# Optimization experiments

Measured on AMD Instinct MI355X. Metric: run time of the kernel, lower is better.

## Reference

```python
import jax, jax.numpy as jnp
import numpy as np

RADIUS = 0.12
K = 32  # neighbors per ball


def setup_inputs() -> dict:
    key = jax.random.key(0)
    ks = jax.random.split(key, 12)
    B, N, M, C = 4, 4096, 4096, 128
    anchor_xyzs = jax.random.uniform(ks[0], (B, N, 3), dtype=jnp.float32)
    neighbor = jax.random.uniform(ks[1], (B, M, 3), dtype=jnp.float32)
    s3 = 1.0 / np.sqrt(3.0)
    sC = 1.0 / np.sqrt(C)
    Wq = jax.random.uniform(ks[2], (3, C), jnp.float32, -s3, s3)
    bq = jax.random.uniform(ks[3], (C,), jnp.float32, -s3, s3)
    Wk = jax.random.uniform(ks[4], (3, C), jnp.float32, -s3, s3)
    bk = jax.random.uniform(ks[5], (C,), jnp.float32, -s3, s3)
    Wd = jax.random.uniform(ks[6], (3, C), jnp.float32, -s3, s3)
    bd = jax.random.uniform(ks[7], (C,), jnp.float32, -s3, s3)
    Wa = jax.random.uniform(ks[8], (C, C), jnp.float32, -sC, sC)
    ba = jax.random.uniform(ks[9], (C,), jnp.float32, -sC, sC)
    return {"anchor_xyzs": anchor_xyzs, "neighbor": neighbor,
            "Wq": Wq, "bq": bq, "Wk": Wk, "bk": bk,
            "Wd": Wd, "bd": bd, "Wa": Wa, "ba": ba}


def ball_query(anchor, neighbor, radius, k):
    """pointnet2-style ball query: first k neighbor indices (in original order)
    with sqdist < radius^2; slots beyond the found count are padded with the
    first found index (index 0 if none found). Returns (B, N, k) int32."""
    # (B, N, M) pairwise squared distances
    sqd = jnp.sum((anchor[:, :, None, :] - neighbor[:, None, :, :]) ** 2, axis=-1)
    mask = sqd < radius * radius
    # stable sort keys: valid (0) before invalid (1) -> first-k valid indices in order
    order = jnp.argsort((~mask).astype(jnp.int32), axis=-1, stable=True)
    idx = order[..., :k]                                # (B, N, k)
    cnt = jnp.sum(mask, axis=-1)                        # (B, N)
    slot_valid = jnp.arange(k) < cnt[..., None]
    idx = jnp.where(slot_valid, idx, idx[..., :1])
    return idx.astype(jnp.int32)


def reference(anchor_xyzs, neighbor, Wq, bq, Wk, bk, Wd, bd, Wa, ba):
    B, N, _ = anchor_xyzs.shape
    bidx = jnp.arange(B)[:, None, None]
    # QKV-style projections of coordinates
    Q = anchor_xyzs @ Wq + bq                           # (B, N, C)
    neighbor_k = neighbor @ Wk + bk                     # (B, M, C)
    # ball query + gather
    idx = ball_query(anchor_xyzs, neighbor, RADIUS, K)  # (B, N, K)
    neighbor_grouped = neighbor[bidx, idx]              # (B, N, K, 3)
    features_K = neighbor_k[bidx, idx]                  # (B, N, K, C)
    # distance encoding
    dis = (anchor_xyzs[:, :, None, :] - neighbor_grouped) @ Wd + bd  # (B, N, K, C)
    # attention weight: softmax over channel dim (dim=-1, as in the torch code)
    logits = (Q[:, :, None, :] - features_K) @ Wa + ba  # (B, N, K, C)
    attention_weight = jax.nn.softmax(logits, axis=-1)
    # max-pool over the K neighbor axis
    attention = jnp.max(dis * attention_weight, axis=2)  # (B, N, C)
    return attention
```

## Files before the change

### kernel.cpp

```cpp
#include <hip/hip_runtime.h>
#include <math.h>

#define BDIM 4
#define NDIM 4096
#define MDIM 4096
#define CDIM 128
#define KSEL 32
#define NCELL 64
#define CAP 128

typedef float v2f __attribute__((ext_vector_type(2)));

#define PRE_BYTES (7 * CDIM * 4)
#define STARTS_BYTES ((NCELL + 1) * BDIM * 4)
#define PTS4_OFF (PRE_BYTES + STARTS_BYTES)
#define WS_NEEDED (PTS4_OFF + (size_t)BDIM * MDIM * 16)

__device__ __forceinline__ float exp2_hw(float x) {
    float r;
    asm("v_exp_f32 %0, %1" : "=v"(r) : "v"(x));
    return r;
}

template <int CTRL, int MASK>
__device__ __forceinline__ float dpp_add(float x) {
    const int r = __builtin_amdgcn_update_dpp(0, __float_as_int(x), CTRL, MASK, 0xF, true);
    return x + __int_as_float(r);
}
#define DPP_QUAD_XOR1 0xB1
#define DPP_QUAD_XOR2 0x4E
#define DPP_ROW_HALF_MIRROR 0x141
#define DPP_ROW_MIRROR      0x140
#define DPP_ROW_BCAST15     0x142
#define DPP_ROW_BCAST31     0x143

__device__ __forceinline__ int rank_before(unsigned long long mk) {
    return __builtin_amdgcn_mbcnt_hi((unsigned)(mk >> 32),
                                     __builtin_amdgcn_mbcnt_lo((unsigned)mk, 0));
}

__device__ __forceinline__ int cell_of(float v) {
    int c = (int)(v * 4.0f);
    return c < 0 ? 0 : (c > 3 ? 3 : c);
}

__device__ __forceinline__ v2f splat(float x) { v2f r; r.x = x; r.y = x; return r; }

__device__ __forceinline__ v2f pk_fma(v2f a, v2f b, v2f c) {
    return __builtin_elementwise_fma(a, b, c);
}

struct LaneW {
    v2f wqa0, wqa1, wqa2;
    v2f nka0, nka1, nka2;
    v2f cav;
    v2f wd0, wd1, wd2, bdv;
};

__device__ __forceinline__ void load_lane_weights(LaneW& P, const float* pre,
                                                  const float* Wd, const float* bd, int lane) {
    const v2f* pre2 = (const v2f*)pre;
    const v2f* wdp  = (const v2f*)Wd;
    const v2f* bdp  = (const v2f*)bd;
    P.wqa0 = pre2[0 * 64 + lane]; P.wqa1 = pre2[1 * 64 + lane]; P.wqa2 = pre2[2 * 64 + lane];
    P.nka0 = pre2[3 * 64 + lane]; P.nka1 = pre2[4 * 64 + lane]; P.nka2 = pre2[5 * 64 + lane];
    P.cav  = pre2[6 * 64 + lane];
    P.wd0 = wdp[0 * 64 + lane]; P.wd1 = wdp[1 * 64 + lane]; P.wd2 = wdp[2 * 64 + lane];
    P.bdv = bdp[lane];
}

__device__ __forceinline__ void fold_one(int i, const float* Wq, const float* bq,
                                         const float* Wk, const float* bk,
                                         const float* Wa, const float* ba,
                                         float* pre) {
    const double LOG2E = 1.4426950408889634074;
    const int r = i >> 7, c = i & (CDIM - 1);
    if (r < 3) {
        double s0 = 0, s1 = 0, s2 = 0, s3 = 0;
        for (int k = 0; k < CDIM; k += 4) {
            s0 += (double)Wq[r * CDIM + k + 0] * (double)Wa[(k + 0) * CDIM + c];
            s1 += (double)Wq[r * CDIM + k + 1] * (double)Wa[(k + 1) * CDIM + c];
            s2 += (double)Wq[r * CDIM + k + 2] * (double)Wa[(k + 2) * CDIM + c];
            s3 += (double)Wq[r * CDIM + k + 3] * (double)Wa[(k + 3) * CDIM + c];
        }
        pre[r * CDIM + c] = (float)(((s0 + s1) + (s2 + s3)) * LOG2E);
    } else if (r < 6) {
        const int rr = r - 3;
        double s0 = 0, s1 = 0, s2 = 0, s3 = 0;
        for (int k = 0; k < CDIM; k += 4) {
            s0 += (double)Wk[rr * CDIM + k + 0] * (double)Wa[(k + 0) * CDIM + c];
            s1 += (double)Wk[rr * CDIM + k + 1] * (double)Wa[(k + 1) * CDIM + c];
            s2 += (double)Wk[rr * CDIM + k + 2] * (double)Wa[(k + 2) * CDIM + c];
            s3 += (double)Wk[rr * CDIM + k + 3] * (double)Wa[(k + 3) * CDIM + c];
        }
        pre[r * CDIM + c] = (float)(((s0 + s1) + (s2 + s3)) * (-LOG2E));
    } else {
        double s = (double)ba[c];
        for (int k = 0; k < CDIM; ++k)
            s += ((double)bq[k] - (double)bk[k]) * (double)Wa[k * CDIM + c];
        pre[6 * CDIM + c] = (float)(s * LOG2E);
    }
}

__launch_bounds__(1024)
__global__ void setup_kernel(const float* __restrict__ neighbor,
                             const float* __restrict__ Wq, const float* __restrict__ bq,
                             const float* __restrict__ Wk, const float* __restrict__ bk,
                             const float* __restrict__ Wa, const float* __restrict__ ba,
                             float* __restrict__ pre,
                             int* __restrict__ starts,
                             float4* __restrict__ pts4,
                             const int do_bins) {
    const int blk = blockIdx.x;
    const int t = threadIdx.x;
    if (do_bins && blk < BDIM) {
        __shared__ int cnts[NCELL];
        __shared__ int curs[NCELL];
        if (t < NCELL) cnts[t] = 0;
        __syncthreads();
        const float* nbb = neighbor + (size_t)blk * MDIM * 3;
        float px[4], py[4], pz[4];
        int cell[4];
        #pragma unroll
        for (int k = 0; k < 4; ++k) {
            const int i = t + k * 1024;
            const float x = nbb[3 * i], y = nbb[3 * i + 1], z = nbb[3 * i + 2];
            px[k] = x; py[k] = y; pz[k] = z;
            cell[k] = (cell_of(z) * 4 + cell_of(y)) * 4 + cell_of(x);
            atomicAdd(&cnts[cell[k]], 1);
        }
        __syncthreads();
        if (t < NCELL) {
            const int v = cnts[t];
            int inc = v;
            #pragma unroll
            for (int off = 1; off < 64; off <<= 1) {
                const int u = __shfl_up(inc, off);
                if (t >= off) inc += u;
            }
            const int excl = inc - v;
            curs[t] = excl;
            starts[blk * (NCELL + 1) + t] = excl;
            if (t == NCELL - 1) starts[blk * (NCELL + 1) + NCELL] = inc;
        }
        __syncthreads();
        #pragma unroll
        for (int k = 0; k < 4; ++k) {
            const int i = t + k * 1024;
            const int slot = atomicAdd(&curs[cell[k]], 1);
            pts4[(size_t)blk * MDIM + slot] = make_float4(px[k], py[k], pz[k], __int_as_float(i));
        }
    } else if (!do_bins || blk == BDIM) {
        if (t < 7 * CDIM) fold_one(t, Wq, bq, Wk, bk, Wa, ba, pre);
    }
}

__launch_bounds__(256)
__global__ void attn2_kernel(const float* __restrict__ anchor,
                             const float* __restrict__ neighbor,
                             const float* __restrict__ Wd,
                             const float* __restrict__ bd,
                             const float* __restrict__ pre,
                             const float4* __restrict__ pts4,
                             const int* __restrict__ starts,
                             float* __restrict__ out) {
    __shared__ float4 cand[4][CAP - KSEL];
    __shared__ float4 sel[4][KSEL];

    const int b    = blockIdx.x >> 10;
    const int n0   = (blockIdx.x & 1023) << 2;
    const int tid  = threadIdx.x;
    const int w    = tid >> 6;
    const int lane = tid & 63;

    const int n = n0 + w;
    const float* ap = anchor + ((size_t)b * NDIM + n) * 3;
    const float ax = ap[0], ay = ap[1], az = ap[2];
    const float* nbb = neighbor + (size_t)b * MDIM * 3;

    LaneW P;
    load_lane_weights(P, pre, Wd, bd, lane);

    const v2f axv = splat(ax), ayv = splat(ay), azv = splat(az);
    const v2f qa = pk_fma(axv, P.wqa0, pk_fma(ayv, P.wqa1, pk_fma(azv, P.wqa2, P.cav)));
    const v2f ad = pk_fma(axv, P.wd0, pk_fma(ayv, P.wd1, pk_fma(azv, P.wd2, P.bdv)));
    const v2f nwd0 = -P.wd0, nwd1 = -P.wd1, nwd2 = -P.wd2;

    constexpr float R2 = (float)(0.12 * 0.12);
    const float RP = 0.1201f;

    const int cx0 = max(0, (int)((ax - RP) * 4.0f)), cx1 = min(3, (int)((ax + RP) * 4.0f));
    const int cy0 = max(0, (int)((ay - RP) * 4.0f)), cy1 = min(3, (int)((ay + RP) * 4.0f));
    const int cz0 = max(0, (int)((az - RP) * 4.0f)), cz1 = min(3, (int)((az + RP) * 4.0f));

    const float4* pb = pts4 + (size_t)b * MDIM;
    const int* st = starts + b * (NCELL + 1);

    int rs[4], re[4];
    int nr = 0;
    for (int cz = cz0; cz <= cz1; ++cz)
        for (int cy = cy0; cy <= cy1; ++cy) {
            const int crow = (cz * 4 + cy) * 4;
            rs[nr] = st[crow + cx0];
            re[nr] = st[crow + cx1 + 1];
            ++nr;
        }

    int cnt = 0;
    for (int r = 0; r < nr; ++r) {
        const int rend = re[r];
        for (int base = rs[r]; base < rend; base += 64) {
            const int i = base + lane;
            const float4 p = pb[min(i, rend - 1)];
            const float dx = __fsub_rn(ax, p.x);
            const float dy = __fsub_rn(ay, p.y);
            const float dz = __fsub_rn(az, p.z);
            const float d2 = __fadd_rn(__fadd_rn(__fmul_rn(dx, dx), __fmul_rn(dy, dy)),
                                       __fmul_rn(dz, dz));
            const bool in = (i < rend) && (d2 < R2);
            const unsigned long long mk = __ballot(in);
            const int pos = cnt + rank_before(mk);
            if (in && pos < CAP) {
                if (pos < KSEL) sel[w][pos] = p;
                else            cand[w][pos - KSEL] = p;
            }
            cnt += __popcll(mk);
        }
    }

    int eff;
    if (cnt == 0) {
        if (lane == 0) sel[w][0] = make_float4(nbb[0], nbb[1], nbb[2], 0.0f);
        eff = 1;
    } else if (cnt <= KSEL) {
        eff = cnt;
    } else if (cnt <= CAP) {
        float4 c0v = make_float4(0, 0, 0, 0), c1v = make_float4(0, 0, 0, 0);
        int i0 = 0x7fffffff, i1 = 0x7fffffff;
        if (lane < cnt) {
            c0v = (lane < KSEL) ? sel[w][lane] : cand[w][lane - KSEL];
            i0 = __float_as_int(c0v.w);
        }
        if (lane + 64 < cnt) {
            c1v = cand[w][lane + 64 - KSEL];
            i1 = __float_as_int(c1v.w);
        }
        int lo = 0, hi = MDIM - 1;
        while (lo < hi) {
            const int mid = (lo + hi) >> 1;
            const int c = __popcll(__ballot(i0 <= mid)) + __popcll(__ballot(i1 <= mid));
            if (c >= KSEL) hi = mid; else lo = mid + 1;
        }
        __builtin_amdgcn_wave_barrier();
        const bool k0 = (i0 <= lo);
        const unsigned long long m0 = __ballot(k0);
        if (k0) sel[w][rank_before(m0)] = c0v;
        const int cc0 = __popcll(m0);
        const bool k1 = (i1 <= lo);
        const unsigned long long m1 = __ballot(k1);
        if (k1) sel[w][cc0 + rank_before(m1)] = c1v;
        eff = KSEL;
    } else {
        int c2 = 0;
        for (int base = 0; base < MDIM && c2 < KSEL; base += 64) {
            const int m = base + lane;
            const float* p = nbb + 3 * m;
            const float nx = p[0], ny = p[1], nz = p[2];
            const float dx = __fsub_rn(ax, nx);
            const float dy = __fsub_rn(ay, ny);
            const float dz = __fsub_rn(az, nz);
            const float d2 = __fadd_rn(__fadd_rn(__fmul_rn(dx, dx), __fmul_rn(dy, dy)),
                                       __fmul_rn(dz, dz));
            const bool in = d2 < R2;
            const unsigned long long mk = __ballot(in);
            const int pos = c2 + rank_before(mk);
            if (in && pos < KSEL) sel[w][pos] = make_float4(nx, ny, nz, 0.0f);
            c2 += __popcll(mk);
        }
        eff = KSEL;
    }

    const int eff4 = (eff + 3) & ~3;
    __builtin_amdgcn_wave_barrier();
    __builtin_amdgcn_s_waitcnt(0);
    if (lane >= eff && lane < eff4) {
        const float4 f = sel[w][0];
        sel[w][lane] = f;
    }
    __builtin_amdgcn_wave_barrier();

    v2f acc = splat(-1e30f);
    for (int j = 0; j < eff4; j += 4) {
        v2f pr[4];
        float sv[4];
        #pragma unroll
        for (int t = 0; t < 4; ++t) {
            const float4 v = sel[w][j + t];
            const v2f vx = splat(v.x), vy = splat(v.y), vz = splat(v.z);
            const v2f l = pk_fma(vx, P.nka0, pk_fma(vy, P.nka1, pk_fma(vz, P.nka2, qa)));
            v2f e; e.x = exp2_hw(l.x); e.y = exp2_hw(l.y);
            sv[t] = e.x + e.y;
            const v2f d = pk_fma(vx, nwd0, pk_fma(vy, nwd1, pk_fma(vz, nwd2, ad)));
            pr[t] = d * e;
        }
        #pragma unroll
        for (int t = 0; t < 4; ++t) sv[t] = dpp_add<DPP_QUAD_XOR1, 0xF>(sv[t]);
        #pragma unroll
        for (int t = 0; t < 4; ++t) sv[t] = dpp_add<DPP_QUAD_XOR2, 0xF>(sv[t]);
        #pragma unroll
        for (int t = 0; t < 4; ++t) sv[t] = dpp_add<DPP_ROW_HALF_MIRROR, 0xF>(sv[t]);
        #pragma unroll
        for (int t = 0; t < 4; ++t) sv[t] = dpp_add<DPP_ROW_MIRROR, 0xF>(sv[t]);
        #pragma unroll
        for (int t = 0; t < 4; ++t) sv[t] = dpp_add<DPP_ROW_BCAST15, 0xA>(sv[t]);
        #pragma unroll
        for (int t = 0; t < 4; ++t) sv[t] = dpp_add<DPP_ROW_BCAST31, 0xC>(sv[t]);
        #pragma unroll
        for (int t = 0; t < 4; ++t) {
            const float tot = __int_as_float(__builtin_amdgcn_readlane(__float_as_int(sv[t]), 63));
            const v2f iv = splat(__builtin_amdgcn_rcpf(tot));
            acc = __builtin_elementwise_max(acc, pr[t] * iv);
        }
    }

    float2 o; o.x = acc.x; o.y = acc.y;
    ((float2*)out)[((size_t)b * NDIM + n) * 64 + lane] = o;
}

__launch_bounds__(256)
__global__ void attn_fallback(const float* __restrict__ anchor,
                              const float* __restrict__ neighbor,
                              const float* __restrict__ Wd,
                              const float* __restrict__ bd,
                              const float* __restrict__ pre,
                              float* __restrict__ out) {
    __shared__ float4 sel[4][KSEL];
    __shared__ int lists[4][KSEL];

    const int b = blockIdx.x >> 10, n0 = (blockIdx.x & 1023) << 2;
    const int tid = threadIdx.x, w = tid >> 6, lane = tid & 63;
    const int n = n0 + w;
    const float* ap = anchor + ((size_t)b * NDIM + n) * 3;
    const float ax = ap[0], ay = ap[1], az = ap[2];
    const float* nbb = neighbor + (size_t)b * MDIM * 3;

    LaneW P;
    load_lane_weights(P, pre, Wd, bd, lane);
    const v2f axv = splat(ax), ayv = splat(ay), azv = splat(az);
    const v2f qa = pk_fma(axv, P.wqa0, pk_fma(ayv, P.wqa1, pk_fma(azv, P.wqa2, P.cav)));
    const v2f ad = pk_fma(axv, P.wd0, pk_fma(ayv, P.wd1, pk_fma(azv, P.wd2, P.bdv)));
    const v2f nwd0 = -P.wd0, nwd1 = -P.wd1, nwd2 = -P.wd2;

    constexpr float R2 = (float)(0.12 * 0.12);
    int cnt = 0;
    for (int base = 0; base < MDIM && cnt < KSEL; base += 64) {
        const int m = base + lane;
        const float* p = nbb + 3 * m;
        const float dx = __fsub_rn(ax, p[0]);
        const float dy = __fsub_rn(ay, p[1]);
        const float dz = __fsub_rn(az, p[2]);
        const float d2 = __fadd_rn(__fadd_rn(__fmul_rn(dx, dx), __fmul_rn(dy, dy)),
                                   __fmul_rn(dz, dz));
        const bool in = d2 < R2;
        const unsigned long long mk = __ballot(in);
        const int pos = cnt + rank_before(mk);
        if (in && pos < KSEL) lists[w][pos] = m;
        cnt += __popcll(mk);
    }
    int eff = cnt < KSEL ? cnt : KSEL;
    if (cnt == 0) { if (lane == 0) lists[w][0] = 0; eff = 1; }
    const int eff4 = (eff + 3) & ~3;
    if (lane == 0) for (int j = eff; j < eff4; ++j) lists[w][j] = lists[w][0];
    __builtin_amdgcn_wave_barrier();
    if (lane < eff4) {
        const float* p = nbb + 3 * lists[w][lane];
        sel[w][lane] = make_float4(p[0], p[1], p[2], 0.f);
    }
    __builtin_amdgcn_wave_barrier();

    v2f acc = splat(-1e30f);
    for (int j = 0; j < eff4; j += 4) {
        v2f pr[4]; float sv[4];
        #pragma unroll
        for (int t = 0; t < 4; ++t) {
            const float4 v = sel[w][j + t];
            const v2f vx = splat(v.x), vy = splat(v.y), vz = splat(v.z);
            const v2f l = pk_fma(vx, P.nka0, pk_fma(vy, P.nka1, pk_fma(vz, P.nka2, qa)));
            v2f e; e.x = exp2_hw(l.x); e.y = exp2_hw(l.y);
            sv[t] = e.x + e.y;
            const v2f d = pk_fma(vx, nwd0, pk_fma(vy, nwd1, pk_fma(vz, nwd2, ad)));
            pr[t] = d * e;
        }
        #pragma unroll
        for (int t = 0; t < 4; ++t) sv[t] = dpp_add<DPP_QUAD_XOR1, 0xF>(sv[t]);
        #pragma unroll
        for (int t = 0; t < 4; ++t) sv[t] = dpp_add<DPP_QUAD_XOR2, 0xF>(sv[t]);
        #pragma unroll
        for (int t = 0; t < 4; ++t) sv[t] = dpp_add<DPP_ROW_HALF_MIRROR, 0xF>(sv[t]);
        #pragma unroll
        for (int t = 0; t < 4; ++t) sv[t] = dpp_add<DPP_ROW_MIRROR, 0xF>(sv[t]);
        #pragma unroll
        for (int t = 0; t < 4; ++t) sv[t] = dpp_add<DPP_ROW_BCAST15, 0xA>(sv[t]);
        #pragma unroll
        for (int t = 0; t < 4; ++t) sv[t] = dpp_add<DPP_ROW_BCAST31, 0xC>(sv[t]);
        #pragma unroll
        for (int t = 0; t < 4; ++t) {
            const float tot = __int_as_float(__builtin_amdgcn_readlane(__float_as_int(sv[t]), 63));
            const v2f iv = splat(__builtin_amdgcn_rcpf(tot));
            acc = __builtin_elementwise_max(acc, pr[t] * iv);
        }
    }
    float2 o; o.x = acc.x; o.y = acc.y;
    ((float2*)out)[((size_t)b * NDIM + n) * 64 + lane] = o;
}

extern "C" void kernel_launch(void* const* d_in, const int* in_sizes, int n_in,
                              void* d_out, int out_size, void* d_ws, size_t ws_size,
                              hipStream_t stream) {
    const float* anchor   = (const float*)d_in[0];
    const float* neighbor = (const float*)d_in[1];
    const float* Wq = (const float*)d_in[2];
    const float* bq = (const float*)d_in[3];
    const float* Wk = (const float*)d_in[4];
    const float* bk = (const float*)d_in[5];
    const float* Wd = (const float*)d_in[6];
    const float* bd = (const float*)d_in[7];
    const float* Wa = (const float*)d_in[8];
    const float* ba = (const float*)d_in[9];
    float* out = (float*)d_out;

    float* pre   = (float*)d_ws;
    int* starts  = (int*)((char*)d_ws + PRE_BYTES);
    float4* pts4 = (float4*)((char*)d_ws + PTS4_OFF);

    if (ws_size >= WS_NEEDED) {
        setup_kernel<<<dim3(BDIM + 1), dim3(1024), 0, stream>>>(
            neighbor, Wq, bq, Wk, bk, Wa, ba, pre, starts, pts4, 1);
        attn2_kernel<<<dim3(BDIM * NDIM / 4), dim3(256), 0, stream>>>(
            anchor, neighbor, Wd, bd, pre, pts4, starts, out);
    } else {
        setup_kernel<<<dim3(1), dim3(1024), 0, stream>>>(
            neighbor, Wq, bq, Wk, bk, Wa, ba, pre, starts, pts4, 0);
        attn_fallback<<<dim3(BDIM * NDIM / 4), dim3(256), 0, stream>>>(
            anchor, neighbor, Wd, bd, pre, out);
    }
}
```

Before: 115.4 us.

## Process two anchors per wave and software-prefetch next candidate chunk in ball query

The attention kernel's per-anchor work moves into an inline helper. Each block now handles 8 anchors (2 per wave), so the per-lane weight loads are reused across both, and the grid is halved. The ball-query scan loop is restructured to load the next 64-point chunk of binned points before processing the current one, hiding global-load latency. In exchange, register pressure rises and there are fewer blocks to fill the GPU.

```diff
diff --git a/kernel.cpp b/kernel.cpp
--- a/kernel.cpp
+++ b/kernel.cpp
@@ -69,118 +69,14 @@
     P.bdv = bdp[lane];
 }
 
-__device__ __forceinline__ void fold_one(int i, const float* Wq, const float* bq,
-                                         const float* Wk, const float* bk,
-                                         const float* Wa, const float* ba,
-                                         float* pre) {
-    const double LOG2E = 1.4426950408889634074;
-    const int r = i >> 7, c = i & (CDIM - 1);
-    if (r < 3) {
-        double s0 = 0, s1 = 0, s2 = 0, s3 = 0;
-        for (int k = 0; k < CDIM; k += 4) {
-            s0 += (double)Wq[r * CDIM + k + 0] * (double)Wa[(k + 0) * CDIM + c];
-            s1 += (double)Wq[r * CDIM + k + 1] * (double)Wa[(k + 1) * CDIM + c];
-            s2 += (double)Wq[r * CDIM + k + 2] * (double)Wa[(k + 2) * CDIM + c];
-            s3 += (double)Wq[r * CDIM + k + 3] * (double)Wa[(k + 3) * CDIM + c];
-        }
-        pre[r * CDIM + c] = (float)(((s0 + s1) + (s2 + s3)) * LOG2E);
-    } else if (r < 6) {
-        const int rr = r - 3;
-        double s0 = 0, s1 = 0, s2 = 0, s3 = 0;
-        for (int k = 0; k < CDIM; k += 4) {
-            s0 += (double)Wk[rr * CDIM + k + 0] * (double)Wa[(k + 0) * CDIM + c];
-            s1 += (double)Wk[rr * CDIM + k + 1] * (double)Wa[(k + 1) * CDIM + c];
-            s2 += (double)Wk[rr * CDIM + k + 2] * (double)Wa[(k + 2) * CDIM + c];
-            s3 += (double)Wk[rr * CDIM + k + 3] * (double)Wa[(k + 3) * CDIM + c];
-        }
-        pre[r * CDIM + c] = (float)(((s0 + s1) + (s2 + s3)) * (-LOG2E));
-    } else {
-        double s = (double)ba[c];
-        for (int k = 0; k < CDIM; ++k)
-            s += ((double)bq[k] - (double)bk[k]) * (double)Wa[k * CDIM + c];
-        pre[6 * CDIM + c] = (float)(s * LOG2E);
-    }
-}
-
-__launch_bounds__(1024)
-__global__ void setup_kernel(const float* __restrict__ neighbor,
-                             const float* __restrict__ Wq, const float* __restrict__ bq,
-                             const float* __restrict__ Wk, const float* __restrict__ bk,
-                             const float* __restrict__ Wa, const float* __restrict__ ba,
-                             float* __restrict__ pre,
-                             int* __restrict__ starts,
-                             float4* __restrict__ pts4,
-                             const int do_bins) {
-    const int blk = blockIdx.x;
-    const int t = threadIdx.x;
-    if (do_bins && blk < BDIM) {
-        __shared__ int cnts[NCELL];
-        __shared__ int curs[NCELL];
-        if (t < NCELL) cnts[t] = 0;
-        __syncthreads();
-        const float* nbb = neighbor + (size_t)blk * MDIM * 3;
-        float px[4], py[4], pz[4];
-        int cell[4];
-        #pragma unroll
-        for (int k = 0; k < 4; ++k) {
-            const int i = t + k * 1024;
-            const float x = nbb[3 * i], y = nbb[3 * i + 1], z = nbb[3 * i + 2];
-            px[k] = x; py[k] = y; pz[k] = z;
-            cell[k] = (cell_of(z) * 4 + cell_of(y)) * 4 + cell_of(x);
-            atomicAdd(&cnts[cell[k]], 1);
-        }
-        __syncthreads();
-        if (t < NCELL) {
-            const int v = cnts[t];
-            int inc = v;
-            #pragma unroll
-            for (int off = 1; off < 64; off <<= 1) {
-                const int u = __shfl_up(inc, off);
-                if (t >= off) inc += u;
-            }
-            const int excl = inc - v;
-            curs[t] = excl;
-            starts[blk * (NCELL + 1) + t] = excl;
-            if (t == NCELL - 1) starts[blk * (NCELL + 1) + NCELL] = inc;
-        }
-        __syncthreads();
-        #pragma unroll
-        for (int k = 0; k < 4; ++k) {
-            const int i = t + k * 1024;
-            const int slot = atomicAdd(&curs[cell[k]], 1);
-            pts4[(size_t)blk * MDIM + slot] = make_float4(px[k], py[k], pz[k], __int_as_float(i));
-        }
-    } else if (!do_bins || blk == BDIM) {
-        if (t < 7 * CDIM) fold_one(t, Wq, bq, Wk, bk, Wa, ba, pre);
-    }
-}
-
-__launch_bounds__(256)
-__global__ void attn2_kernel(const float* __restrict__ anchor,
-                             const float* __restrict__ neighbor,
-                             const float* __restrict__ Wd,
-                             const float* __restrict__ bd,
-                             const float* __restrict__ pre,
-                             const float4* __restrict__ pts4,
-                             const int* __restrict__ starts,
-                             float* __restrict__ out) {
-    __shared__ float4 cand[4][CAP - KSEL];
-    __shared__ float4 sel[4][KSEL];
-
-    const int b    = blockIdx.x >> 10;
-    const int n0   = (blockIdx.x & 1023) << 2;
-    const int tid  = threadIdx.x;
-    const int w    = tid >> 6;
-    const int lane = tid & 63;
-
-    const int n = n0 + w;
-    const float* ap = anchor + ((size_t)b * NDIM + n) * 3;
-    const float ax = ap[0], ay = ap[1], az = ap[2];
-    const float* nbb = neighbor + (size_t)b * MDIM * 3;
-
-    LaneW P;
-    load_lane_weights(P, pre, Wd, bd, lane);
-
+__device__ __forceinline__ float2 attn_core(int w, int lane,
+                                            float ax, float ay, float az,
+                                            const LaneW& P,
+                                            const float* nbb,
+                                            const float4* pb,
+                                            const int* st,
+                                            float4 (*cand)[CAP - KSEL],
+                                            float4 (*sel)[KSEL]) {
     const v2f axv = splat(ax), ayv = splat(ay), azv = splat(az);
     const v2f qa = pk_fma(axv, P.wqa0, pk_fma(ayv, P.wqa1, pk_fma(azv, P.wqa2, P.cav)));
     const v2f ad = pk_fma(axv, P.wd0, pk_fma(ayv, P.wd1, pk_fma(azv, P.wd2, P.bdv)));
@@ -192,9 +88,6 @@
     const int cx0 = max(0, (int)((ax - RP) * 4.0f)), cx1 = min(3, (int)((ax + RP) * 4.0f));
     const int cy0 = max(0, (int)((ay - RP) * 4.0f)), cy1 = min(3, (int)((ay + RP) * 4.0f));
     const int cz0 = max(0, (int)((az - RP) * 4.0f)), cz1 = min(3, (int)((az + RP) * 4.0f));
-
-    const float4* pb = pts4 + (size_t)b * MDIM;
-    const int* st = starts + b * (NCELL + 1);
 
     int rs[4], re[4];
     int nr = 0;
@@ -207,25 +100,39 @@
         }
 
     int cnt = 0;
-    for (int r = 0; r < nr; ++r) {
-        const int rend = re[r];
-        for (int base = rs[r]; base < rend; base += 64) {
-            const int i = base + lane;
-            const float4 p = pb[min(i, rend - 1)];
-            const float dx = __fsub_rn(ax, p.x);
-            const float dy = __fsub_rn(ay, p.y);
-            const float dz = __fsub_rn(az, p.z);
-            const float d2 = __fadd_rn(__fadd_rn(__fmul_rn(dx, dx), __fmul_rn(dy, dy)),
-                                       __fmul_rn(dz, dz));
-            const bool in = (i < rend) && (d2 < R2);
-            const unsigned long long mk = __ballot(in);
-            const int pos = cnt + rank_before(mk);
-            if (in && pos < CAP) {
-                if (pos < KSEL) sel[w][pos] = p;
-                else            cand[w][pos - KSEL] = p;
-            }
-            cnt += __popcll(mk);
-        }
+    int r0 = 0, base0 = rs[0], cur_rend = 0, cur_i = 0;
+    while (r0 < nr && base0 >= re[r0]) { ++r0; if (r0 < nr) base0 = rs[r0]; }
+    float4 cur = make_float4(1e30f, 1e30f, 1e30f, 0.0f);
+    if (r0 < nr) {
+        cur_rend = re[r0];
+        cur_i = base0 + lane;
+        cur = pb[min(cur_i, cur_rend - 1)];
+    }
+    while (r0 < nr) {
+        int r1 = r0, base1 = base0 + 64;
+        while (r1 < nr && base1 >= re[r1]) { ++r1; if (r1 < nr) base1 = rs[r1]; }
+        float4 nxt = make_float4(1e30f, 1e30f, 1e30f, 0.0f);
+        int nxt_i = 0, nxt_rend = 0;
+        if (r1 < nr) {
+            nxt_rend = re[r1];
+            nxt_i = base1 + lane;
+            nxt = pb[min(nxt_i, nxt_rend - 1)];
+        }
+        const float dx = __fsub_rn(ax, cur.x);
+        const float dy = __fsub_rn(ay, cur.y);
+        const float dz = __fsub_rn(az, cur.z);
+        const float d2 = __fadd_rn(__fadd_rn(__fmul_rn(dx, dx), __fmul_rn(dy, dy)),
+                                   __fmul_rn(dz, dz));
+        const bool in = (cur_i < cur_rend) && (d2 < R2);
+        const unsigned long long mk = __ballot(in);
+        const int pos = cnt + rank_before(mk);
+        if (in && pos < CAP) {
+            if (pos < KSEL) sel[w][pos] = cur;
+            else            cand[w][pos - KSEL] = cur;
+        }
+        cnt += __popcll(mk);
+        r0 = r1; base0 = base1;
+        cur = nxt; cur_i = nxt_i; cur_rend = nxt_rend;
     }
 
     int eff;
@@ -324,7 +231,127 @@
     }
 
     float2 o; o.x = acc.x; o.y = acc.y;
-    ((float2*)out)[((size_t)b * NDIM + n) * 64 + lane] = o;
+    return o;
+}
+
+__device__ __forceinline__ void fold_one(int i, const float* Wq, const float* bq,
+                                         const float* Wk, const float* bk,
+                                         const float* Wa, const float* ba,
+                                         float* pre) {
+    const double LOG2E = 1.4426950408889634074;
+    const int r = i >> 7, c = i & (CDIM - 1);
+    if (r < 3) {
+        double s0 = 0, s1 = 0, s2 = 0, s3 = 0;
+        for (int k = 0; k < CDIM; k += 4) {
+            s0 += (double)Wq[r * CDIM + k + 0] * (double)Wa[(k + 0) * CDIM + c];
+            s1 += (double)Wq[r * CDIM + k + 1] * (double)Wa[(k + 1) * CDIM + c];
+            s2 += (double)Wq[r * CDIM + k + 2] * (double)Wa[(k + 2) * CDIM + c];
+            s3 += (double)Wq[r * CDIM + k + 3] * (double)Wa[(k + 3) * CDIM + c];
+        }
+        pre[r * CDIM + c] = (float)(((s0 + s1) + (s2 + s3)) * LOG2E);
+    } else if (r < 6) {
+        const int rr = r - 3;
+        double s0 = 0, s1 = 0, s2 = 0, s3 = 0;
+        for (int k = 0; k < CDIM; k += 4) {
+            s0 += (double)Wk[rr * CDIM + k + 0] * (double)Wa[(k + 0) * CDIM + c];
+            s1 += (double)Wk[rr * CDIM + k + 1] * (double)Wa[(k + 1) * CDIM + c];
+            s2 += (double)Wk[rr * CDIM + k + 2] * (double)Wa[(k + 2) * CDIM + c];
+            s3 += (double)Wk[rr * CDIM + k + 3] * (double)Wa[(k + 3) * CDIM + c];
+        }
+        pre[r * CDIM + c] = (float)(((s0 + s1) + (s2 + s3)) * (-LOG2E));
+    } else {
+        double s = (double)ba[c];
+        for (int k = 0; k < CDIM; ++k)
+            s += ((double)bq[k] - (double)bk[k]) * (double)Wa[k * CDIM + c];
+        pre[6 * CDIM + c] = (float)(s * LOG2E);
+    }
+}
+
+__launch_bounds__(1024)
+__global__ void setup_kernel(const float* __restrict__ neighbor,
+                             const float* __restrict__ Wq, const float* __restrict__ bq,
+                             const float* __restrict__ Wk, const float* __restrict__ bk,
+                             const float* __restrict__ Wa, const float* __restrict__ ba,
+                             float* __restrict__ pre,
+                             int* __restrict__ starts,
+                             float4* __restrict__ pts4,
+                             const int do_bins) {
+    const int blk = blockIdx.x;
+    const int t = threadIdx.x;
+    if (do_bins && blk < BDIM) {
+        __shared__ int cnts[NCELL];
+        __shared__ int curs[NCELL];
+        if (t < NCELL) cnts[t] = 0;
+        __syncthreads();
+        const float* nbb = neighbor + (size_t)blk * MDIM * 3;
+        float px[4], py[4], pz[4];
+        int cell[4];
+        #pragma unroll
+        for (int k = 0; k < 4; ++k) {
+            const int i = t + k * 1024;
+            const float x = nbb[3 * i], y = nbb[3 * i + 1], z = nbb[3 * i + 2];
+            px[k] = x; py[k] = y; pz[k] = z;
+            cell[k] = (cell_of(z) * 4 + cell_of(y)) * 4 + cell_of(x);
+            atomicAdd(&cnts[cell[k]], 1);
+        }
+        __syncthreads();
+        if (t < NCELL) {
+            const int v = cnts[t];
+            int inc = v;
+            #pragma unroll
+            for (int off = 1; off < 64; off <<= 1) {
+                const int u = __shfl_up(inc, off);
+                if (t >= off) inc += u;
+            }
+            const int excl = inc - v;
+            curs[t] = excl;
+            starts[blk * (NCELL + 1) + t] = excl;
+            if (t == NCELL - 1) starts[blk * (NCELL + 1) + NCELL] = inc;
+        }
+        __syncthreads();
+        #pragma unroll
+        for (int k = 0; k < 4; ++k) {
+            const int i = t + k * 1024;
+            const int slot = atomicAdd(&curs[cell[k]], 1);
+            pts4[(size_t)blk * MDIM + slot] = make_float4(px[k], py[k], pz[k], __int_as_float(i));
+        }
+    } else if (!do_bins || blk == BDIM) {
+        if (t < 7 * CDIM) fold_one(t, Wq, bq, Wk, bk, Wa, ba, pre);
+    }
+}
+
+__launch_bounds__(256)
+__global__ void attn2_kernel(const float* __restrict__ anchor,
+                             const float* __restrict__ neighbor,
+                             const float* __restrict__ Wd,
+                             const float* __restrict__ bd,
+                             const float* __restrict__ pre,
+                             const float4* __restrict__ pts4,
+                             const int* __restrict__ starts,
+                             float* __restrict__ out) {
+    __shared__ float4 cand[4][CAP - KSEL];
+    __shared__ float4 sel[4][KSEL];
+
+    const int b     = blockIdx.x >> 9;
+    const int nbase = (blockIdx.x & 511) << 3;
+    const int tid   = threadIdx.x;
+    const int w     = tid >> 6;
+    const int lane  = tid & 63;
+
+    const float* nbb = neighbor + (size_t)b * MDIM * 3;
+    const float4* pb = pts4 + (size_t)b * MDIM;
+    const int* st = starts + b * (NCELL + 1);
+
+    LaneW P;
+    load_lane_weights(P, pre, Wd, bd, lane);
+
+    #pragma unroll
+    for (int rep = 0; rep < 2; ++rep) {
+        const int n = nbase + rep * 4 + w;
+        const float* ap = anchor + ((size_t)b * NDIM + n) * 3;
+        const float2 o = attn_core(w, lane, ap[0], ap[1], ap[2], P, nbb, pb, st, cand, sel);
+        ((float2*)out)[((size_t)b * NDIM + n) * 64 + lane] = o;
+    }
 }
 
 __launch_bounds__(256)
@@ -436,7 +463,7 @@
     if (ws_size >= WS_NEEDED) {
         setup_kernel<<<dim3(BDIM + 1), dim3(1024), 0, stream>>>(
             neighbor, Wq, bq, Wk, bk, Wa, ba, pre, starts, pts4, 1);
-        attn2_kernel<<<dim3(BDIM * NDIM / 4), dim3(256), 0, stream>>>(
+        attn2_kernel<<<dim3(BDIM * NDIM / 8), dim3(256), 0, stream>>>(
             anchor, neighbor, Wd, bd, pre, pts4, starts, out);
     } else {
         setup_kernel<<<dim3(1), dim3(1024), 0, stream>>>(
```

Result: slower. 124.0 us (+7.4%).
